# Kernel tuning notes

Measured on AMD Instinct MI355X. Metric: run time of the kernel, lower is better.

The kernel has to match this reference:

```python
import jax, jax.numpy as jnp
import numpy as np

N_QUBITS = 9
N_LAYERS = 4
EPS = 1e-5


def _apply_ry(state, wire, theta):
    # state: [N, 2**n] real; theta: [N] or scalar
    n = N_QUBITS
    N = state.shape[0]
    left, right = 2 ** wire, 2 ** (n - 1 - wire)
    s = state.reshape(N, left, 2, right)
    th = jnp.broadcast_to(jnp.asarray(theta, state.dtype), (N,))[:, None, None]
    c, si = jnp.cos(th / 2), jnp.sin(th / 2)
    a, b = s[:, :, 0, :], s[:, :, 1, :]
    out = jnp.stack([c * a - si * b, si * a + c * b], axis=2)
    return out.reshape(N, -1)


def _apply_cnot(state, ctrl, tgt):
    n = N_QUBITS
    N = state.shape[0]
    s = state.reshape((N,) + (2,) * n)
    ca, ta = ctrl + 1, tgt + 1
    sub = jnp.take(s, 1, axis=ca)          # control == 1 slice
    ta2 = ta - 1 if ta > ca else ta
    sub = jnp.flip(sub, axis=ta2)          # X on target
    idx = [slice(None)] * (n + 1)
    idx[ca] = 1
    s = s.at[tuple(idx)].set(sub)
    return s.reshape(N, -1)


def quantum_layer(inputs, q_weights):
    # inputs: [N, n_qubits] angles; q_weights: [n_layers, n_qubits]
    N = inputs.shape[0]
    state = jnp.zeros((N, 2 ** N_QUBITS), inputs.dtype).at[:, 0].set(1.0)
    for i in range(N_QUBITS):
        state = _apply_ry(state, i, inputs[:, i])
    for j in range(N_LAYERS):
        for i in range(N_QUBITS):
            state = _apply_cnot(state, i, (i + 1) % N_QUBITS)
        for i in range(N_QUBITS):
            state = _apply_ry(state, i, q_weights[j, i])
    probs = (state * state).reshape((N,) + (2,) * N_QUBITS)
    zs = []
    for i in range(N_QUBITS):
        axes = tuple(a for a in range(1, N_QUBITS + 1) if a != i + 1)
        p = probs.sum(axes)                # [N, 2]
        zs.append(p[:, 0] - p[:, 1])
    return jnp.stack(zs, axis=1)           # [N, n_qubits]


def _bn(x):
    mu = x.mean((0, 2, 3), keepdims=True)
    var = x.var((0, 2, 3), keepdims=True)
    return (x - mu) * jax.lax.rsqrt(var + EPS)


def _maxpool(x, kh, kw):
    return jax.lax.reduce_window(x, -jnp.inf, jax.lax.max,
                                 (1, 1, kh, kw), (1, 1, kh, kw), 'VALID')


def _conv(x, w):
    return jax.lax.conv_general_dilated(x, w, (1, 1), 'VALID',
                                        dimension_numbers=('NCHW', 'OIHW', 'NCHW'))


def _forward(x, w_conv1, w_conv2, w_conv3, q_weights, fc_w, fc_b):
    h = jax.nn.elu(_bn(_conv(x, w_conv1)))
    h = jnp.pad(h, ((0, 0), (0, 0), (0, 1), (16, 17)))     # ZeroPad2d(16,17,0,1)
    h = _maxpool(jax.nn.elu(_bn(_conv(h, w_conv2))), 2, 4)
    h = jnp.pad(h, ((0, 0), (0, 0), (4, 3), (2, 1)))       # ZeroPad2d(2,1,4,3)
    h = _maxpool(jax.nn.elu(_bn(_conv(h, w_conv3))), 2, 4)
    B, C = h.shape[0], h.shape[1]
    feats = h.reshape(B, C, -1)                            # [B, 32, 9]
    q = quantum_layer(feats.reshape(B * C, N_QUBITS), q_weights)
    q = q.reshape(B, C * N_QUBITS)                         # channel-major concat
    return q @ fc_w.T + fc_b


def setup_inputs() -> dict:
    key = jax.random.key(0)
    ks = jax.random.split(key, 7)
    return {
        'x': jax.random.normal(ks[0], (1024, 1, 4, 216), jnp.float32),
        'w_conv1': jax.random.normal(ks[1], (16, 1, 1, 64), jnp.float32) * 0.05,
        'w_conv2': jax.random.normal(ks[2], (32, 16, 2, 32), jnp.float32) * 0.05,
        'w_conv3': jax.random.normal(ks[3], (32, 32, 8, 4), jnp.float32) * 0.05,
        'q_weights': jax.random.uniform(ks[4], (N_LAYERS, N_QUBITS), jnp.float32, 0.0, 2 * np.pi),
        'fc_w': jax.random.normal(ks[5], (5, 32 * N_QUBITS), jnp.float32) * 0.05,
        'fc_b': jnp.zeros((5,), jnp.float32),
    }


def reference(x, w_conv1, w_conv2, w_conv3, q_weights, fc_w, fc_b):
    return _forward(x, w_conv1, w_conv2, w_conv3, q_weights, fc_w, fc_b)
```

## Files before the change

kernel.cpp:

```cpp
#include <hip/hip_runtime.h>
#include <math.h>

#define NB 1024
#define C1 16
#define H1 4
#define W1 153
#define WX 216
#define K1 64
#define C2 32
#define H2 4
#define W2 155
#define W192 192
#define PW2 38
#define C3 32
#define W3 38

typedef short short4v __attribute__((ext_vector_type(4)));
typedef short short8 __attribute__((ext_vector_type(8)));
typedef float f32x16 __attribute__((ext_vector_type(16)));

#define OFF_OUT1     0
#define OFF_A1H      10027008
#define OFF_A1L      16318464
#define OFF_W2PH     22609920
#define OFF_W2PL     22626304
#define OFF_W3PH     22642688
#define OFF_W3PL     22659072
#define OFF_UH       22675456
#define OFF_UL       22806528
#define OFF_POOL2RAW 22937600
#define OFF_A2H      25427968
#define OFF_A2L      27787264
#define OFF_FEATSRAW 30146560
#define OFF_QO       30441472
#define OFF_PART1    30736384
#define OFF_PART2    30867456
#define OFF_PART3    30998528
#define OFF_STATS1   31031296
#define OFF_STATS2   31031328
#define OFF_STATS3   31031392

__device__ __forceinline__ float eluf(float x){ return x > 0.f ? x : expm1f(x); }

__device__ __forceinline__ ushort bf16h(float x){
  unsigned u = __float_as_uint(x);
  unsigned r = u + 0x7fffu + ((u >> 16) & 1u);
  return (ushort)(r >> 16);
}
__device__ __forceinline__ float bf16f(ushort h){ return __uint_as_float(((unsigned)h) << 16); }

__device__ __forceinline__ short8 cat8(short4v a, short4v b){
  return __builtin_shufflevector(a, b, 0,1,2,3,4,5,6,7);
}

__global__ __launch_bounds__(256) void k_conv1s(const float* __restrict__ x,
                                                const float* __restrict__ w1,
                                                float* __restrict__ out1,
                                                float* __restrict__ part1){
  __shared__ float xr[4][WX];
  __shared__ float wl[C1*K1];
  int n = blockIdx.x, tid = threadIdx.x;
  for (int i = tid; i < 4*WX; i += 256) xr[i/WX][i%WX] = x[(size_t)n*4*WX + i];
  for (int i = tid; i < C1*K1; i += 256) wl[i] = w1[i];
  __syncthreads();
  int h = tid >> 6, lane = tid & 63;
  float acc[16][3];
  #pragma unroll
  for (int c = 0; c < 16; ++c){ acc[c][0]=0.f; acc[c][1]=0.f; acc[c][2]=0.f; }
  bool v2 = (lane + 128) < W1;
  for (int k = 0; k < 64; ++k){
    float x0 = xr[h][lane + k];
    float x1 = xr[h][lane + 64 + k];
    float x2 = v2 ? xr[h][lane + 128 + k] : 0.f;
    #pragma unroll
    for (int c = 0; c < 16; ++c){
      float wk = wl[c*64 + k];
      acc[c][0] += wk*x0; acc[c][1] += wk*x1; acc[c][2] += wk*x2;
    }
  }
  float ss[16], sq[16];
  #pragma unroll
  for (int c = 0; c < 16; ++c){
    float* ob = out1 + (((size_t)(n*16 + c)*4 + h))*W1;
    ob[lane] = acc[c][0];
    ob[lane + 64] = acc[c][1];
    if (v2) ob[lane + 128] = acc[c][2];
    ss[c] = acc[c][0] + acc[c][1] + acc[c][2];
    sq[c] = acc[c][0]*acc[c][0] + acc[c][1]*acc[c][1] + acc[c][2]*acc[c][2];
  }
  #pragma unroll
  for (int m = 1; m < 64; m <<= 1){
    #pragma unroll
    for (int c = 0; c < 16; ++c){ ss[c] += __shfl_xor(ss[c], m); sq[c] += __shfl_xor(sq[c], m); }
  }
  if (lane == 0){
    #pragma unroll
    for (int c = 0; c < 16; ++c){
      part1[((size_t)(n*4 + h)*16 + c)*2]     = ss[c];
      part1[((size_t)(n*4 + h)*16 + c)*2 + 1] = sq[c];
    }
  }
}

__global__ __launch_bounds__(256) void k_stats_finP(const float* __restrict__ part,
                                                    float* __restrict__ stats,
                                                    int C, int nblk, float inv){
  __shared__ float rs[256], rq[256];
  int c = blockIdx.x;
  float s = 0.f, q = 0.f;
  for (int b = threadIdx.x; b < nblk; b += 256){
    s += part[((size_t)b*C + c)*2];
    q += part[((size_t)b*C + c)*2 + 1];
  }
  rs[threadIdx.x] = s; rq[threadIdx.x] = q; __syncthreads();
  for (int st = 128; st > 0; st >>= 1){
    if (threadIdx.x < st){ rs[threadIdx.x] += rs[threadIdx.x+st]; rq[threadIdx.x] += rq[threadIdx.x+st]; }
    __syncthreads();
  }
  if (threadIdx.x == 0){
    float mean = rs[0]*inv;
    float var  = rq[0]*inv - mean*mean;
    stats[c*2]   = mean;
    stats[c*2+1] = rsqrtf(var + 1e-5f);
  }
}

__global__ __launch_bounds__(256) void k_bnelu1(const float* __restrict__ out1,
                                                const float* __restrict__ stats,
                                                ushort* __restrict__ a1h, ushort* __restrict__ a1l){
  __shared__ float xf[2448];
  __shared__ float st[32];
  int b = blockIdx.x;
  int n = b >> 2, h = b & 3;
  int tid = threadIdx.x;
  if (tid < 32) st[tid] = stats[tid];
  for (int i = tid; i < 2448; i += 256){
    int ci = i / 153, w = i - ci*153;
    xf[i] = out1[((size_t)(n*16 + ci)*4 + h)*W1 + w];
  }
  __syncthreads();
  for (int i = tid; i < 3072; i += 256){
    int w = i >> 4, ci = i & 15;
    float v = 0.f;
    int ws = w - 16;
    if ((unsigned)ws < (unsigned)W1){
      float xx = xf[ci*153 + ws];
      v = eluf((xx - st[ci*2])*st[ci*2+1]);
    }
    int ciS = ci ^ (((w >> 2) & 3) << 2);
    size_t o = (size_t)b*3072 + w*16 + ciS;
    ushort hs = bf16h(v);
    a1h[o] = hs;
    a1l[o] = bf16h(v - bf16f(hs));
  }
}

__global__ void k_cvtw(const float* __restrict__ w2, const float* __restrict__ w3,
                       ushort* __restrict__ w2ph, ushort* __restrict__ w2pl,
                       ushort* __restrict__ w3ph, ushort* __restrict__ w3pl){
  int idx = blockIdx.x*256 + threadIdx.x;
  if (idx < 32768){
    int ci = idx & 15; int co = (idx >> 4) & 31; int rk = idx >> 9;
    int r = rk >> 5, kw = rk & 31;
    float v = w2[((size_t)(co*16 + ci)*2 + r)*32 + kw];
    ushort hs = bf16h(v); float hf = bf16f(hs);
    w2ph[idx] = hs; w2pl[idx] = bf16h(v - hf);
  } else {
    int j = idx - 32768;
    int ci = j & 31; int co = (j >> 5) & 31; int rk = j >> 10;
    int r = rk >> 2, kw = rk & 3;
    float v = w3[((size_t)(co*32 + ci)*8 + r)*4 + kw];
    ushort hs = bf16h(v); float hf = bf16f(hs);
    w3ph[j] = hs; w3pl[j] = bf16h(v - hf);
  }
}

__global__ __launch_bounds__(128) void k_conv2f(const ushort* __restrict__ a1h,
                                                const ushort* __restrict__ a1l,
                                                const ushort* __restrict__ w2ph,
                                                const ushort* __restrict__ w2pl,
                                                float* __restrict__ pool2raw,
                                                float* __restrict__ part2){
  __shared__ __align__(16) ushort s_hi[3*3072];
  __shared__ __align__(16) ushort s_lo[3*3072];
  __shared__ float statL[2][32][2];
  float* poolF = (float*)s_hi;
  int b = blockIdx.x;
  int n = b >> 1, ph = b & 1;
  int tid = threadIdx.x;
  int row0 = 2*ph;
  int nrows = ph ? 2 : 3;
  {
    const float4* gh = (const float4*)(a1h + ((size_t)n*4 + row0)*3072);
    const float4* gl = (const float4*)(a1l + ((size_t)n*4 + row0)*3072);
    float4* dh = (float4*)s_hi;
    float4* dl = (float4*)s_lo;
    int cnt = nrows*384;
    for (int i = tid; i < cnt; i += 128){ dh[i] = gh[i]; dl[i] = gl[i]; }
  }
  __syncthreads();
  int wv = tid >> 6, lane = tid & 63;
  int h = 2*ph + wv;
  int l5 = lane >> 5, l31 = lane & 31;

  f32x16 acc[5];
  #pragma unroll
  for (int p = 0; p < 5; ++p)
    #pragma unroll
    for (int e = 0; e < 16; ++e) acc[p][e] = 0.f;

  int rmax = (h == 3) ? 1 : 2;
  for (int r = 0; r < rmax; ++r){
    int rb = (wv + r)*3072;
    for (int kw = 0; kw < 32; ++kw){
      int widx = (((r << 5) + kw)*32 + l31)*16 + l5*4;
      short8 Ah = cat8(*(const short4v*)(w2ph + widx), *(const short4v*)(w2ph + widx + 8));
      short8 Al = cat8(*(const short4v*)(w2pl + widx), *(const short4v*)(w2pl + widx + 8));
      short8 Bh[5], Bl[5];
      #pragma unroll
      for (int p = 0; p < 5; ++p){
        int pos = p*32 + l31 + kw;
        int sw = ((pos >> 2) & 3) << 2;
        int off0 = rb + pos*16 + ((l5*4) ^ sw);
        int off1 = rb + pos*16 + ((l5*4 + 8) ^ sw);
        Bh[p] = cat8(*(const short4v*)(s_hi + off0), *(const short4v*)(s_hi + off1));
        Bl[p] = cat8(*(const short4v*)(s_lo + off0), *(const short4v*)(s_lo + off1));
      }
      #pragma unroll
      for (int p = 0; p < 5; ++p) acc[p] = __builtin_amdgcn_mfma_f32_32x32x16_bf16(Ah, Bh[p], acc[p], 0, 0, 0);
      #pragma unroll
      for (int p = 0; p < 5; ++p) acc[p] = __builtin_amdgcn_mfma_f32_32x32x16_bf16(Ah, Bl[p], acc[p], 0, 0, 0);
      #pragma unroll
      for (int p = 0; p < 5; ++p) acc[p] = __builtin_amdgcn_mfma_f32_32x32x16_bf16(Al, Bh[p], acc[p], 0, 0, 0);
    }
  }
  __syncthreads();

  {
    float sreg[16], qreg[16];
    #pragma unroll
    for (int e = 0; e < 16; ++e){ sreg[e] = 0.f; qreg[e] = 0.f; }
    #pragma unroll
    for (int p = 0; p < 5; ++p){
      bool pv = (p < 4) || (l31 < 27);
      #pragma unroll
      for (int e = 0; e < 16; ++e){
        float v = pv ? acc[p][e] : 0.f;
        sreg[e] += v; qreg[e] += v*v;
      }
    }
    #pragma unroll
    for (int m = 1; m < 32; m <<= 1){
      #pragma unroll
      for (int e = 0; e < 16; ++e){
        sreg[e] += __shfl_xor(sreg[e], m);
        qreg[e] += __shfl_xor(qreg[e], m);
      }
    }
    if (l31 == 0){
      #pragma unroll
      for (int e = 0; e < 16; ++e){
        int co = (e & 3) + ((e >> 2) << 3) + (l5 << 2);
        statL[wv][co][0] = sreg[e];
        statL[wv][co][1] = qreg[e];
      }
    }
  }
  #pragma unroll
  for (int p = 0; p < 5; ++p){
    #pragma unroll
    for (int e = 0; e < 16; ++e){
      float v = acc[p][e];
      float v1 = fmaxf(v, __shfl_xor(v, 1));
      float v2m = fmaxf(v1, __shfl_xor(v1, 2));
      int pw = p*8 + (l31 >> 2);
      if ((l31 & 3) == 0 && pw < PW2){
        int co = (e & 3) + ((e >> 2) << 3) + (l5 << 2);
        poolF[(wv*32 + co)*40 + pw] = v2m;
      }
    }
  }
  __syncthreads();
  for (int i = tid; i < 32*PW2; i += 128){
    int pw = i % PW2; int co = i / PW2;
    float v = fmaxf(poolF[co*40 + pw], poolF[(32 + co)*40 + pw]);
    pool2raw[(((size_t)n*2 + ph)*32 + co)*PW2 + pw] = v;
  }
  if (tid < 32){
    float s = statL[0][tid][0] + statL[1][tid][0];
    float q = statL[0][tid][1] + statL[1][tid][1];
    part2[((size_t)(n*2 + ph)*32 + tid)*2]     = s;
    part2[((size_t)(n*2 + ph)*32 + tid)*2 + 1] = q;
  }
}

__global__ __launch_bounds__(256) void k_bn2(const float* __restrict__ pool2raw,
                                             const float* __restrict__ stats,
                                             ushort* __restrict__ a2h, ushort* __restrict__ a2l){
  __shared__ float xf[1216];
  __shared__ float st[64];
  int b = blockIdx.x;
  int tid = threadIdx.x;
  if (tid < 64) st[tid] = stats[tid];
  for (int i = tid; i < 1216; i += 256) xf[i] = pool2raw[(size_t)b*1216 + i];
  __syncthreads();
  for (int i = tid; i < 2304; i += 256){
    int w = i >> 5, ci = i & 31;
    float v = 0.f;
    int pw = w - 2;
    if ((unsigned)pw < (unsigned)PW2)
      v = eluf((xf[ci*38 + pw] - st[ci*2])*st[ci*2+1]);
    int ciS = ci ^ (((w >> 1) & 7) << 2);
    size_t o = (size_t)b*2304 + w*32 + ciS;
    ushort hs = bf16h(v);
    a2h[o] = hs; a2l[o] = bf16h(v - bf16f(hs));
  }
}

__global__ __launch_bounds__(256, 2) void k_conv3f(const ushort* __restrict__ a2h,
                                                   const ushort* __restrict__ a2l,
                                                   const ushort* __restrict__ w3ph,
                                                   const ushort* __restrict__ w3pl,
                                                   float* __restrict__ featsraw,
                                                   float* __restrict__ part3){
  __shared__ __align__(16) ushort s3h[9216];
  __shared__ __align__(16) ushort s3l[9216];
  __shared__ float poolL3[4][32][12];
  __shared__ float statL3[4][32][2];
  int nb = blockIdx.x;
  int tid = threadIdx.x;
  {
    const float4* gh = (const float4*)(a2h + (size_t)nb*9216);
    const float4* gl = (const float4*)(a2l + (size_t)nb*9216);
    float4* dh = (float4*)s3h;
    float4* dl = (float4*)s3l;
    for (int i = tid; i < 1152; i += 256){ dh[i] = gh[i]; dl[i] = gl[i]; }
  }
  __syncthreads();
  int wave = tid >> 6, lane = tid & 63;
  int nh = wave >> 1, h = wave & 1;
  int l5 = lane >> 5, l31 = lane & 31;

  f32x16 acc[2];
  #pragma unroll
  for (int p = 0; p < 2; ++p)
    #pragma unroll
    for (int e = 0; e < 16; ++e) acc[p][e] = 0.f;

  #pragma unroll
  for (int ri = 0; ri < 2; ++ri){
    int r = (h == 0) ? (4 + ri) : (3 + ri);
    int rbase = (nh*2 + ri)*72*32;
    #pragma unroll
    for (int kw = 0; kw < 4; ++kw){
      #pragma unroll
      for (int ch = 0; ch < 2; ++ch){
        int widx = ((r*4 + kw)*32 + l31)*32 + ch*16 + l5*4;
        short8 Ah = cat8(*(const short4v*)(w3ph + widx), *(const short4v*)(w3ph + widx + 8));
        short8 Al = cat8(*(const short4v*)(w3pl + widx), *(const short4v*)(w3pl + widx + 8));
        short8 Bh[2], Bl[2];
        #pragma unroll
        for (int p = 0; p < 2; ++p){
          int pos = p*32 + l31 + kw;
          int sw = ((pos >> 1) & 7) << 2;
          int s0 = ch*16 + l5*4;
          int off0 = rbase + pos*32 + (s0 ^ sw);
          int off1 = rbase + pos*32 + ((s0 + 8) ^ sw);
          Bh[p] = cat8(*(const short4v*)(s3h + off0), *(const short4v*)(s3h + off1));
          Bl[p] = cat8(*(const short4v*)(s3l + off0), *(const short4v*)(s3l + off1));
        }
        #pragma unroll
        for (int p = 0; p < 2; ++p) acc[p] = __builtin_amdgcn_mfma_f32_32x32x16_bf16(Ah, Bh[p], acc[p], 0, 0, 0);
        #pragma unroll
        for (int p = 0; p < 2; ++p) acc[p] = __builtin_amdgcn_mfma_f32_32x32x16_bf16(Ah, Bl[p], acc[p], 0, 0, 0);
        #pragma unroll
        for (int p = 0; p < 2; ++p) acc[p] = __builtin_amdgcn_mfma_f32_32x32x16_bf16(Al, Bh[p], acc[p], 0, 0, 0);
      }
    }
  }

  {
    float sreg[16], qreg[16];
    #pragma unroll
    for (int e = 0; e < 16; ++e){ sreg[e] = 0.f; qreg[e] = 0.f; }
    #pragma unroll
    for (int p = 0; p < 2; ++p){
      bool pv = (p == 0) || (l31 < 6);
      #pragma unroll
      for (int e = 0; e < 16; ++e){
        float v = pv ? acc[p][e] : 0.f;
        sreg[e] += v; qreg[e] += v*v;
      }
    }
    #pragma unroll
    for (int m = 1; m < 32; m <<= 1){
      #pragma unroll
      for (int e = 0; e < 16; ++e){
        sreg[e] += __shfl_xor(sreg[e], m);
        qreg[e] += __shfl_xor(qreg[e], m);
      }
    }
    if (l31 == 0){
      #pragma unroll
      for (int e = 0; e < 16; ++e){
        int co = (e & 3) + ((e >> 2) << 3) + (l5 << 2);
        statL3[wave][co][0] = sreg[e];
        statL3[wave][co][1] = qreg[e];
      }
    }
  }
  #pragma unroll
  for (int p = 0; p < 2; ++p){
    #pragma unroll
    for (int e = 0; e < 16; ++e){
      float v = acc[p][e];
      float v1 = fmaxf(v, __shfl_xor(v, 1));
      float v2m = fmaxf(v1, __shfl_xor(v1, 2));
      int pw = p*8 + (l31 >> 2);
      if ((l31 & 3) == 0 && pw < 9){
        int co = (e & 3) + ((e >> 2) << 3) + (l5 << 2);
        poolL3[wave][co][pw] = v2m;
      }
    }
  }
  __syncthreads();
  for (int i = tid; i < 2*32*9; i += 256){
    int pw = i % 9; int t = i / 9; int co = t & 31; int nh2 = t >> 5;
    float v = fmaxf(poolL3[nh2*2][co][pw], poolL3[nh2*2+1][co][pw]);
    featsraw[((size_t)(nb*2 + nh2)*32 + co)*9 + pw] = v;
  }
  if (tid < 32){
    float s = 0.f, q = 0.f;
    #pragma unroll
    for (int wv = 0; wv < 4; ++wv){ s += statL3[wv][tid][0]; q += statL3[wv][tid][1]; }
    part3[((size_t)nb*32 + tid)*2]     = s;
    part3[((size_t)nb*32 + tid)*2 + 1] = q;
  }
}

__global__ __launch_bounds__(256) void k_buildU(const float* __restrict__ qw,
                                                ushort* __restrict__ Uh, ushort* __restrict__ Ul){
  __shared__ float wt[36][2];
  int tid = threadIdx.x;
  if (tid < 36){ float s, c; sincosf(qw[tid]*0.5f, &s, &c); wt[tid][0] = c; wt[tid][1] = s; }
  __syncthreads();
  int wid = tid >> 6, lane = tid & 63;
  int k = blockIdx.x*4 + wid;
  float v[8];
  #pragma unroll
  for (int r = 0; r < 8; ++r) v[r] = (lane*8 + r == k) ? 1.f : 0.f;

  for (int j = 0; j < 4; ++j){
    #pragma unroll
    for (int i = 0; i < 5; ++i){
      int cm = 32>>i, tm = 16>>i;
      bool flip = (lane & cm) != 0;
      #pragma unroll
      for (int r = 0; r < 8; ++r){
        float w = __shfl_xor(v[r], tm);
        v[r] = flip ? w : v[r];
      }
    }
    { bool flip = (lane & 1) != 0;
      #pragma unroll
      for (int r = 0; r < 4; ++r){ float a = v[r], bb = v[r+4]; v[r] = flip?bb:a; v[r+4] = flip?a:bb; } }
    { float t = v[4]; v[4] = v[6]; v[6] = t; t = v[5]; v[5] = v[7]; v[7] = t; }
    { float t = v[2]; v[2] = v[3]; v[3] = t; t = v[6]; v[6] = v[7]; v[7] = t; }
    #pragma unroll
    for (int r = 1; r < 8; r += 2) v[r] = __shfl_xor(v[r], 32);

    #pragma unroll
    for (int i = 0; i < 6; ++i){
      float c = wt[j*9+i][0], s = wt[j*9+i][1];
      int m = 32>>i;
      float sg = (lane & m) ? s : -s;
      #pragma unroll
      for (int r = 0; r < 8; ++r){
        float w = __shfl_xor(v[r], m);
        v[r] = c*v[r] + sg*w;
      }
    }
    { float c = wt[j*9+6][0], s = wt[j*9+6][1];
      #pragma unroll
      for (int r = 0; r < 4; ++r){ float a = v[r], bb = v[r+4]; v[r] = c*a - s*bb; v[r+4] = s*a + c*bb; } }
    { float c = wt[j*9+7][0], s = wt[j*9+7][1]; float a, bb;
      a=v[0]; bb=v[2]; v[0]=c*a-s*bb; v[2]=s*a+c*bb;
      a=v[1]; bb=v[3]; v[1]=c*a-s*bb; v[3]=s*a+c*bb;
      a=v[4]; bb=v[6]; v[4]=c*a-s*bb; v[6]=s*a+c*bb;
      a=v[5]; bb=v[7]; v[5]=c*a-s*bb; v[7]=s*a+c*bb; }
    { float c = wt[j*9+8][0], s = wt[j*9+8][1]; float a, bb;
      a=v[0]; bb=v[1]; v[0]=c*a-s*bb; v[1]=s*a+c*bb;
      a=v[2]; bb=v[3]; v[2]=c*a-s*bb; v[3]=s*a+c*bb;
      a=v[4]; bb=v[5]; v[4]=c*a-s*bb; v[5]=s*a+c*bb;
      a=v[6]; bb=v[7]; v[6]=c*a-s*bb; v[7]=s*a+c*bb; }
  }
  #pragma unroll
  for (int r = 0; r < 8; ++r){
    int s = lane*8 + r;
    int mf = s >> 5, r31 = s & 31;
    int addr = (((k >> 4)*16 + mf)*32 + r31)*16 + (k & 15);
    float f = v[r];
    ushort hi = bf16h(f);
    Uh[addr] = hi;
    Ul[addr] = bf16h(f - bf16f(hi));
  }
}

__global__ __launch_bounds__(256, 1) void k_qgemm(const float* __restrict__ featsraw,
                                                  const float* __restrict__ stats,
                                                  const ushort* __restrict__ Uh,
                                                  const ushort* __restrict__ Ul,
                                                  float* __restrict__ qo){
  __shared__ __align__(16) ushort BhL[32768];
  __shared__ __align__(16) ushort BlL[32768];
  __shared__ float angL[576];
  __shared__ float zred[4][64][9];
  int nb = blockIdx.x;
  int tid = threadIdx.x;
  for (int t = tid; t < 576; t += 256){
    float vr = featsraw[(size_t)nb*576 + t];
    int c = (t/9) & 31;
    angL[t] = 0.5f * eluf((vr - stats[c*2])*stats[c*2+1]);
  }
  __syncthreads();
  {
    int sm = tid >> 2, q = tid & 3;
    float tc[9], ts[9];
    #pragma unroll
    for (int i = 0; i < 9; ++i) sincosf(angL[sm*9 + i], &ts[i], &tc[i]);
    float Pc = ((q & 2) ? ts[0] : tc[0]) * ((q & 1) ? ts[1] : tc[1]);
    int swz = (sm >> 2) & 3;
    short4v* bh4 = (short4v*)BhL;
    short4v* bl4 = (short4v*)BlL;
    int j = 0;
    #pragma unroll
    for (int b2 = 0; b2 < 2; ++b2){ float p2 = Pc*(b2 ? ts[2] : tc[2]);
    #pragma unroll
    for (int b3 = 0; b3 < 2; ++b3){ float p3 = p2*(b3 ? ts[3] : tc[3]);
    #pragma unroll
    for (int b4 = 0; b4 < 2; ++b4){ float p4 = p3*(b4 ? ts[4] : tc[4]);
    #pragma unroll
    for (int b5 = 0; b5 < 2; ++b5){ float p5 = p4*(b5 ? ts[5] : tc[5]);
    #pragma unroll
    for (int b6 = 0; b6 < 2; ++b6){ float p6 = p5*(b6 ? ts[6] : tc[6]);
      float a0 = p6*tc[7]*tc[8];
      float a1 = p6*tc[7]*ts[8];
      float a2 = p6*ts[7]*tc[8];
      float a3 = p6*ts[7]*ts[8];
      ushort h0 = bf16h(a0), h1 = bf16h(a1), h2 = bf16h(a2), h3 = bf16h(a3);
      short4v hv; hv[0]=(short)h0; hv[1]=(short)h1; hv[2]=(short)h2; hv[3]=(short)h3;
      short4v lv; lv[0]=(short)bf16h(a0 - bf16f(h0)); lv[1]=(short)bf16h(a1 - bf16f(h1));
                  lv[2]=(short)bf16h(a2 - bf16f(h2)); lv[3]=(short)bf16h(a3 - bf16f(h3));
      int kk = q*128 + j;
      int kstep = kk >> 4;
      int g = (kk >> 2) & 3;
      int idx4 = (kstep*64 + sm)*4 + (g ^ swz);
      bh4[idx4] = hv; bl4[idx4] = lv;
      j += 4;
    }}}}}
  }
  __syncthreads();
  int wv = tid >> 6, lane = tid & 63, l5 = lane >> 5, l31 = lane & 31;
  f32x16 acc[4][2];
  #pragma unroll
  for (int jj = 0; jj < 4; ++jj)
    #pragma unroll
    for (int nf = 0; nf < 2; ++nf)
      #pragma unroll
      for (int e = 0; e < 16; ++e) acc[jj][nf][e] = 0.f;

  for (int kstep = 0; kstep < 32; ++kstep){
    short8 Bh[2], Bl[2];
    #pragma unroll
    for (int nf = 0; nf < 2; ++nf){
      int sm = nf*32 + l31;
      int base = (kstep*64 + sm)*16;
      int sz = ((sm >> 2) & 3) << 2;
      int e0 = (l5*4) ^ sz;
      int e1 = (l5*4 + 8) ^ sz;
      Bh[nf] = cat8(*(const short4v*)(BhL + base + e0), *(const short4v*)(BhL + base + e1));
      Bl[nf] = cat8(*(const short4v*)(BlL + base + e0), *(const short4v*)(BlL + base + e1));
    }
    #pragma unroll
    for (int jj = 0; jj < 4; ++jj){
      int mf = wv*4 + jj;
      const ushort* ah = Uh + ((kstep*16 + mf)*32 + l31)*16 + l5*4;
      const ushort* al = Ul + ((kstep*16 + mf)*32 + l31)*16 + l5*4;
      short8 Ah = cat8(*(const short4v*)ah, *(const short4v*)(ah + 8));
      short8 Al = cat8(*(const short4v*)al, *(const short4v*)(al + 8));
      acc[jj][0] = __builtin_amdgcn_mfma_f32_32x32x16_bf16(Ah, Bh[0], acc[jj][0], 0, 0, 0);
      acc[jj][1] = __builtin_amdgcn_mfma_f32_32x32x16_bf16(Ah, Bh[1], acc[jj][1], 0, 0, 0);
      acc[jj][0] = __builtin_amdgcn_mfma_f32_32x32x16_bf16(Ah, Bl[0], acc[jj][0], 0, 0, 0);
      acc[jj][1] = __builtin_amdgcn_mfma_f32_32x32x16_bf16(Ah, Bl[1], acc[jj][1], 0, 0, 0);
      acc[jj][0] = __builtin_amdgcn_mfma_f32_32x32x16_bf16(Al, Bh[0], acc[jj][0], 0, 0, 0);
      acc[jj][1] = __builtin_amdgcn_mfma_f32_32x32x16_bf16(Al, Bh[1], acc[jj][1], 0, 0, 0);
    }
  }
  float zz[2][9];
  #pragma unroll
  for (int nf = 0; nf < 2; ++nf)
    #pragma unroll
    for (int i = 0; i < 9; ++i) zz[nf][i] = 0.f;
  #pragma unroll
  for (int jj = 0; jj < 4; ++jj){
    int mf = wv*4 + jj;
    float sg0 = (mf & 8) ? -1.f : 1.f;
    float sg1 = (mf & 4) ? -1.f : 1.f;
    float sg2 = (mf & 2) ? -1.f : 1.f;
    float sg3 = (mf & 1) ? -1.f : 1.f;
    #pragma unroll
    for (int nf = 0; nf < 2; ++nf){
      float psum = 0.f, z4 = 0.f, z5 = 0.f, z7 = 0.f, z8 = 0.f;
      #pragma unroll
      for (int e = 0; e < 16; ++e){
        float qv = acc[jj][nf][e]*acc[jj][nf][e];
        psum += qv;
        z4 += ((e >> 3) & 1) ? -qv : qv;
        z5 += ((e >> 2) & 1) ? -qv : qv;
        z7 += ((e >> 1) & 1) ? -qv : qv;
        z8 += (e & 1) ? -qv : qv;
      }
      zz[nf][0] += sg0*psum; zz[nf][1] += sg1*psum;
      zz[nf][2] += sg2*psum; zz[nf][3] += sg3*psum;
      zz[nf][4] += z4; zz[nf][5] += z5;
      zz[nf][6] += l5 ? -psum : psum;
      zz[nf][7] += z7; zz[nf][8] += z8;
    }
  }
  #pragma unroll
  for (int nf = 0; nf < 2; ++nf)
    #pragma unroll
    for (int i = 0; i < 9; ++i) zz[nf][i] += __shfl_xor(zz[nf][i], 32);
  if (l5 == 0){
    #pragma unroll
    for (int nf = 0; nf < 2; ++nf)
      #pragma unroll
      for (int i = 0; i < 9; ++i) zred[wv][nf*32 + l31][i] = zz[nf][i];
  }
  __syncthreads();
  for (int t = tid; t < 576; t += 256){
    int sm = t / 9, i = t - sm*9;
    float s = zred[0][sm][i] + zred[1][sm][i] + zred[2][sm][i] + zred[3][sm][i];
    qo[(size_t)(nb*64 + sm)*9 + i] = s;
  }
}

__global__ void k_fc(const float* __restrict__ q, const float* __restrict__ fw,
                     const float* __restrict__ fb, float* __restrict__ out){
  int idx = blockIdx.x*256 + threadIdx.x;
  if (idx >= NB*5) return;
  int b = idx / 5, o = idx - b*5;
  const float* qr = q + (size_t)b*288;
  const float* wr = fw + (size_t)o*288;
  float s = 0.f;
  for (int j = 0; j < 288; ++j) s += qr[j]*wr[j];
  out[idx] = s + fb[o];
}

extern "C" void kernel_launch(void* const* d_in, const int* in_sizes, int n_in,
                              void* d_out, int out_size, void* d_ws, size_t ws_size,
                              hipStream_t stream){
  const float* x  = (const float*)d_in[0];
  const float* w1 = (const float*)d_in[1];
  const float* w2 = (const float*)d_in[2];
  const float* w3 = (const float*)d_in[3];
  const float* qw = (const float*)d_in[4];
  const float* fw = (const float*)d_in[5];
  const float* fb = (const float*)d_in[6];
  float* out = (float*)d_out;
  float* W = (float*)d_ws;

  float*  out1   = W + OFF_OUT1;
  ushort* a1h    = (ushort*)(W + OFF_A1H);
  ushort* a1l    = (ushort*)(W + OFF_A1L);
  ushort* w2ph   = (ushort*)(W + OFF_W2PH);
  ushort* w2pl   = (ushort*)(W + OFF_W2PL);
  ushort* w3ph   = (ushort*)(W + OFF_W3PH);
  ushort* w3pl   = (ushort*)(W + OFF_W3PL);
  ushort* uH     = (ushort*)(W + OFF_UH);
  ushort* uL     = (ushort*)(W + OFF_UL);
  float*  pool2raw = W + OFF_POOL2RAW;
  ushort* a2h    = (ushort*)(W + OFF_A2H);
  ushort* a2l    = (ushort*)(W + OFF_A2L);
  float*  featsraw = W + OFF_FEATSRAW;
  float*  qo     = W + OFF_QO;
  float*  part1  = W + OFF_PART1;
  float*  part2  = W + OFF_PART2;
  float*  part3  = W + OFF_PART3;
  float*  stats1 = W + OFF_STATS1;
  float*  stats2 = W + OFF_STATS2;
  float*  stats3 = W + OFF_STATS3;

  k_conv1s<<<NB, 256, 0, stream>>>(x, w1, out1, part1);
  k_stats_finP<<<16, 256, 0, stream>>>(part1, stats1, 16, NB*4, 1.f/((float)NB*H1*W1));
  k_bnelu1<<<NB*4, 256, 0, stream>>>(out1, stats1, a1h, a1l);
  k_cvtw<<<256, 256, 0, stream>>>(w2, w3, w2ph, w2pl, w3ph, w3pl);
  k_buildU<<<128, 256, 0, stream>>>(qw, uH, uL);
  k_conv2f<<<NB*2, 128, 0, stream>>>(a1h, a1l, w2ph, w2pl, pool2raw, part2);
  k_stats_finP<<<32, 256, 0, stream>>>(part2, stats2, 32, NB*2, 1.f/((float)NB*H2*W2));
  k_bn2<<<NB*2, 256, 0, stream>>>(pool2raw, stats2, a2h, a2l);
  k_conv3f<<<NB/2, 256, 0, stream>>>(a2h, a2l, w3ph, w3pl, featsraw, part3);
  k_stats_finP<<<32, 256, 0, stream>>>(part3, stats3, 32, NB/2, 1.f/((float)NB*2*W3));
  k_qgemm<<<NB/2, 256, 0, stream>>>(featsraw, stats3, uH, uL, qo);
  k_fc<<<20, 256, 0, stream>>>(qo, fw, fb, out);
}
```

Baseline: 376.5 us.

## Restructure conv2 so each wave owns a pooled row pair and position slice

The conv2 kernel now runs one 256-thread block per sample instead of two 128-thread blocks. Each of the four waves handles a pooled-row group and a subset of output positions, and accumulates both input rows of the height pool in registers. The height max-pool now happens in registers, which removes the shared-memory pool staging and an extra barrier. Each kernel weight fragment is reused across the two input rows, and the whole sample's activations are loaded once. In exchange the kernel uses more LDS per block and more accumulator registers per wave, and the wave roles are skewed by sample index to spread the uneven work.

```diff
diff --git a/kernel.cpp b/kernel.cpp
--- a/kernel.cpp
+++ b/kernel.cpp
@@ -175,122 +175,147 @@
   }
 }
 
-__global__ __launch_bounds__(128) void k_conv2f(const ushort* __restrict__ a1h,
+template<int HG, int PS>
+__device__ __forceinline__ void conv2_body(const ushort* s_hi, const ushort* s_lo,
+                                           const ushort* __restrict__ w2ph,
+                                           const ushort* __restrict__ w2pl,
+                                           float* __restrict__ pool2raw,
+                                           float (*statW)[32][2],
+                                           int n, int l31, int l5){
+  constexpr int P0 = PS ? 3 : 0;
+  constexpr int NP = PS ? 2 : 3;
+  constexpr int NR = (HG == 0) ? 3 : 2;
+
+  f32x16 acc[2][NP];
+  #pragma unroll
+  for (int lh = 0; lh < 2; ++lh)
+    #pragma unroll
+    for (int p = 0; p < NP; ++p)
+      #pragma unroll
+      for (int e = 0; e < 16; ++e) acc[lh][p][e] = 0.f;
+
+  for (int kw = 0; kw < 32; ++kw){
+    short8 Ah[2], Al[2];
+    #pragma unroll
+    for (int r = 0; r < 2; ++r){
+      int widx = ((r*32 + kw)*32 + l31)*16 + l5*4;
+      Ah[r] = cat8(*(const short4v*)(w2ph + widx), *(const short4v*)(w2ph + widx + 8));
+      Al[r] = cat8(*(const short4v*)(w2pl + widx), *(const short4v*)(w2pl + widx + 8));
+    }
+    #pragma unroll
+    for (int j = 0; j < NR; ++j){
+      int rb = (2*HG + j)*3072;
+      short8 bh[NP], bl[NP];
+      #pragma unroll
+      for (int p = 0; p < NP; ++p){
+        int pos = (P0 + p)*32 + l31 + kw;
+        int sw = ((pos >> 2) & 3) << 2;
+        int off0 = rb + pos*16 + ((l5*4) ^ sw);
+        int off1 = rb + pos*16 + ((l5*4 + 8) ^ sw);
+        bh[p] = cat8(*(const short4v*)(s_hi + off0), *(const short4v*)(s_hi + off1));
+        bl[p] = cat8(*(const short4v*)(s_lo + off0), *(const short4v*)(s_lo + off1));
+      }
+      #pragma unroll
+      for (int lh = 0; lh < 2; ++lh){
+        #pragma unroll
+        for (int r = 0; r < 2; ++r){
+          if (lh + r != j) continue;
+          #pragma unroll
+          for (int p = 0; p < NP; ++p){
+            acc[lh][p] = __builtin_amdgcn_mfma_f32_32x32x16_bf16(Ah[r], bh[p], acc[lh][p], 0, 0, 0);
+            acc[lh][p] = __builtin_amdgcn_mfma_f32_32x32x16_bf16(Ah[r], bl[p], acc[lh][p], 0, 0, 0);
+            acc[lh][p] = __builtin_amdgcn_mfma_f32_32x32x16_bf16(Al[r], bh[p], acc[lh][p], 0, 0, 0);
+          }
+        }
+      }
+    }
+  }
+
+  {
+    float sreg[16], qreg[16];
+    #pragma unroll
+    for (int e = 0; e < 16; ++e){ sreg[e] = 0.f; qreg[e] = 0.f; }
+    #pragma unroll
+    for (int lh = 0; lh < 2; ++lh){
+      #pragma unroll
+      for (int p = 0; p < NP; ++p){
+        bool pv = ((P0 + p) < 4) || (l31 < 27);
+        #pragma unroll
+        for (int e = 0; e < 16; ++e){
+          float v = pv ? acc[lh][p][e] : 0.f;
+          sreg[e] += v; qreg[e] += v*v;
+        }
+      }
+    }
+    #pragma unroll
+    for (int m = 1; m < 32; m <<= 1){
+      #pragma unroll
+      for (int e = 0; e < 16; ++e){
+        sreg[e] += __shfl_xor(sreg[e], m);
+        qreg[e] += __shfl_xor(qreg[e], m);
+      }
+    }
+    if (l31 == 0){
+      #pragma unroll
+      for (int e = 0; e < 16; ++e){
+        int co = (e & 3) + ((e >> 2) << 3) + (l5 << 2);
+        statW[HG*2 + PS][co][0] = sreg[e];
+        statW[HG*2 + PS][co][1] = qreg[e];
+      }
+    }
+  }
+  #pragma unroll
+  for (int p = 0; p < NP; ++p){
+    #pragma unroll
+    for (int e = 0; e < 16; ++e){
+      float m0 = fmaxf(acc[0][p][e], acc[1][p][e]);
+      float v1 = fmaxf(m0, __shfl_xor(m0, 1));
+      float v2m = fmaxf(v1, __shfl_xor(v1, 2));
+      int pw = (P0 + p)*8 + (l31 >> 2);
+      if ((l31 & 3) == 0 && pw < PW2){
+        int co = (e & 3) + ((e >> 2) << 3) + (l5 << 2);
+        pool2raw[(((size_t)n*2 + HG)*32 + co)*PW2 + pw] = v2m;
+      }
+    }
+  }
+}
+
+__global__ __launch_bounds__(256) void k_conv2f(const ushort* __restrict__ a1h,
                                                 const ushort* __restrict__ a1l,
                                                 const ushort* __restrict__ w2ph,
                                                 const ushort* __restrict__ w2pl,
                                                 float* __restrict__ pool2raw,
                                                 float* __restrict__ part2){
-  __shared__ __align__(16) ushort s_hi[3*3072];
-  __shared__ __align__(16) ushort s_lo[3*3072];
-  __shared__ float statL[2][32][2];
-  float* poolF = (float*)s_hi;
-  int b = blockIdx.x;
-  int n = b >> 1, ph = b & 1;
+  __shared__ __align__(16) ushort s_hi[4*3072];
+  __shared__ __align__(16) ushort s_lo[4*3072];
+  __shared__ float statW[4][32][2];
+  int n = blockIdx.x;
   int tid = threadIdx.x;
-  int row0 = 2*ph;
-  int nrows = ph ? 2 : 3;
   {
-    const float4* gh = (const float4*)(a1h + ((size_t)n*4 + row0)*3072);
-    const float4* gl = (const float4*)(a1l + ((size_t)n*4 + row0)*3072);
+    const float4* gh = (const float4*)(a1h + (size_t)n*12288);
+    const float4* gl = (const float4*)(a1l + (size_t)n*12288);
     float4* dh = (float4*)s_hi;
     float4* dl = (float4*)s_lo;
-    int cnt = nrows*384;
-    for (int i = tid; i < cnt; i += 128){ dh[i] = gh[i]; dl[i] = gl[i]; }
+    #pragma unroll
+    for (int i = 0; i < 6; ++i){ dh[tid + 256*i] = gh[tid + 256*i]; dl[tid + 256*i] = gl[tid + 256*i]; }
   }
   __syncthreads();
   int wv = tid >> 6, lane = tid & 63;
-  int h = 2*ph + wv;
   int l5 = lane >> 5, l31 = lane & 31;
-
-  f32x16 acc[5];
-  #pragma unroll
-  for (int p = 0; p < 5; ++p)
-    #pragma unroll
-    for (int e = 0; e < 16; ++e) acc[p][e] = 0.f;
-
-  int rmax = (h == 3) ? 1 : 2;
-  for (int r = 0; r < rmax; ++r){
-    int rb = (wv + r)*3072;
-    for (int kw = 0; kw < 32; ++kw){
-      int widx = (((r << 5) + kw)*32 + l31)*16 + l5*4;
-      short8 Ah = cat8(*(const short4v*)(w2ph + widx), *(const short4v*)(w2ph + widx + 8));
-      short8 Al = cat8(*(const short4v*)(w2pl + widx), *(const short4v*)(w2pl + widx + 8));
-      short8 Bh[5], Bl[5];
-      #pragma unroll
-      for (int p = 0; p < 5; ++p){
-        int pos = p*32 + l31 + kw;
-        int sw = ((pos >> 2) & 3) << 2;
-        int off0 = rb + pos*16 + ((l5*4) ^ sw);
-        int off1 = rb + pos*16 + ((l5*4 + 8) ^ sw);
-        Bh[p] = cat8(*(const short4v*)(s_hi + off0), *(const short4v*)(s_hi + off1));
-        Bl[p] = cat8(*(const short4v*)(s_lo + off0), *(const short4v*)(s_lo + off1));
-      }
-      #pragma unroll
-      for (int p = 0; p < 5; ++p) acc[p] = __builtin_amdgcn_mfma_f32_32x32x16_bf16(Ah, Bh[p], acc[p], 0, 0, 0);
-      #pragma unroll
-      for (int p = 0; p < 5; ++p) acc[p] = __builtin_amdgcn_mfma_f32_32x32x16_bf16(Ah, Bl[p], acc[p], 0, 0, 0);
-      #pragma unroll
-      for (int p = 0; p < 5; ++p) acc[p] = __builtin_amdgcn_mfma_f32_32x32x16_bf16(Al, Bh[p], acc[p], 0, 0, 0);
-    }
-  }
-  __syncthreads();
-
-  {
-    float sreg[16], qreg[16];
-    #pragma unroll
-    for (int e = 0; e < 16; ++e){ sreg[e] = 0.f; qreg[e] = 0.f; }
-    #pragma unroll
-    for (int p = 0; p < 5; ++p){
-      bool pv = (p < 4) || (l31 < 27);
-      #pragma unroll
-      for (int e = 0; e < 16; ++e){
-        float v = pv ? acc[p][e] : 0.f;
-        sreg[e] += v; qreg[e] += v*v;
-      }
-    }
-    #pragma unroll
-    for (int m = 1; m < 32; m <<= 1){
-      #pragma unroll
-      for (int e = 0; e < 16; ++e){
-        sreg[e] += __shfl_xor(sreg[e], m);
-        qreg[e] += __shfl_xor(qreg[e], m);
-      }
-    }
-    if (l31 == 0){
-      #pragma unroll
-      for (int e = 0; e < 16; ++e){
-        int co = (e & 3) + ((e >> 2) << 3) + (l5 << 2);
-        statL[wv][co][0] = sreg[e];
-        statL[wv][co][1] = qreg[e];
-      }
-    }
-  }
-  #pragma unroll
-  for (int p = 0; p < 5; ++p){
-    #pragma unroll
-    for (int e = 0; e < 16; ++e){
-      float v = acc[p][e];
-      float v1 = fmaxf(v, __shfl_xor(v, 1));
-      float v2m = fmaxf(v1, __shfl_xor(v1, 2));
-      int pw = p*8 + (l31 >> 2);
-      if ((l31 & 3) == 0 && pw < PW2){
-        int co = (e & 3) + ((e >> 2) << 3) + (l5 << 2);
-        poolF[(wv*32 + co)*40 + pw] = v2m;
-      }
-    }
-  }
-  __syncthreads();
-  for (int i = tid; i < 32*PW2; i += 128){
-    int pw = i % PW2; int co = i / PW2;
-    float v = fmaxf(poolF[co*40 + pw], poolF[(32 + co)*40 + pw]);
-    pool2raw[(((size_t)n*2 + ph)*32 + co)*PW2 + pw] = v;
-  }
-  if (tid < 32){
-    float s = statL[0][tid][0] + statL[1][tid][0];
-    float q = statL[0][tid][1] + statL[1][tid][1];
-    part2[((size_t)(n*2 + ph)*32 + tid)*2]     = s;
-    part2[((size_t)(n*2 + ph)*32 + tid)*2 + 1] = q;
+  int role = (wv + n) & 3;
+  switch (role){
+    case 0: conv2_body<0,0>(s_hi, s_lo, w2ph, w2pl, pool2raw, statW, n, l31, l5); break;
+    case 1: conv2_body<0,1>(s_hi, s_lo, w2ph, w2pl, pool2raw, statW, n, l31, l5); break;
+    case 2: conv2_body<1,0>(s_hi, s_lo, w2ph, w2pl, pool2raw, statW, n, l31, l5); break;
+    default: conv2_body<1,1>(s_hi, s_lo, w2ph, w2pl, pool2raw, statW, n, l31, l5); break;
+  }
+  __syncthreads();
+  if (tid < 64){
+    int hg = tid >> 5, co = tid & 31;
+    float s = statW[hg*2][co][0] + statW[hg*2 + 1][co][0];
+    float q = statW[hg*2][co][1] + statW[hg*2 + 1][co][1];
+    part2[(((size_t)n*2 + hg)*32 + co)*2]     = s;
+    part2[(((size_t)n*2 + hg)*32 + co)*2 + 1] = q;
   }
 }
 
@@ -696,7 +721,7 @@
   k_bnelu1<<<NB*4, 256, 0, stream>>>(out1, stats1, a1h, a1l);
   k_cvtw<<<256, 256, 0, stream>>>(w2, w3, w2ph, w2pl, w3ph, w3pl);
   k_buildU<<<128, 256, 0, stream>>>(qw, uH, uL);
-  k_conv2f<<<NB*2, 128, 0, stream>>>(a1h, a1l, w2ph, w2pl, pool2raw, part2);
+  k_conv2f<<<NB, 256, 0, stream>>>(a1h, a1l, w2ph, w2pl, pool2raw, part2);
   k_stats_finP<<<32, 256, 0, stream>>>(part2, stats2, 32, NB*2, 1.f/((float)NB*H2*W2));
   k_bn2<<<NB*2, 256, 0, stream>>>(pool2raw, stats2, a2h, a2l);
   k_conv3f<<<NB/2, 256, 0, stream>>>(a2h, a2l, w3ph, w3pl, featsraw, part3);
```

Measured after the change: 338.2 us. -10.1%, faster.
